# Performance work log

Hardware: AMD Instinct MI355X
Metric: run time of the kernel (lower is better)

## Reference

```python
import jax, jax.numpy as jnp
import numpy as np

B, C, H, W = 8, 256, 32, 32
N_HEADS, CH = 8, 32          # channel_head = channels // num_heads
HID = N_HEADS * CH           # hidden_channels


def setup_inputs() -> dict:
    key = jax.random.key(0)
    k1, k2, k3 = jax.random.split(key, 3)
    return {
        "x": jax.random.normal(k1, (B, C, H, W), dtype=jnp.float32),
        "w_qkv": jax.random.normal(k2, (3 * HID, C), dtype=jnp.float32) * 0.02,
        "b_qkv": jnp.zeros((3 * HID,), dtype=jnp.float32),
        "w_out": jax.random.normal(k3, (C, HID), dtype=jnp.float32) * 0.02,
        "b_out": jnp.zeros((C,), dtype=jnp.float32),
    }


def reference(x, w_qkv, b_qkv, w_out, b_out):
    b, c, h, w = x.shape
    s = h * w
    # qkv_conv: 1x1 conv + SiLU (norm='none' inside Conv2dBlock)
    qkv = jnp.einsum('bchw,oc->bohw', x, w_qkv) + b_qkv[None, :, None, None]
    qkv = jax.nn.silu(qkv)
    # rearrange 'b (n c) h w -> b n (3*ch) s' then chunk into q,k,v
    qkv = qkv.reshape(b, N_HEADS, 3 * CH, s)
    q, k, v = jnp.split(qkv, 3, axis=2)          # each [b, n, ch, s]
    # scores over flattened spatial positions, scaled by sqrt(channel_head)
    scores = jnp.einsum('bncs,bnct->bnst', q, k) / jnp.sqrt(jnp.float32(CH))
    attn = jax.nn.softmax(scores, axis=-1)        # softmax over key positions
    out = jnp.einsum('bnst,bnct->bncs', attn, v)  # [b, n, ch, s]
    out = out.reshape(b, N_HEADS * CH, h, w)      # 'b n c h w -> b (n c) h w'
    # out_conv: 1x1 conv, activation='none'
    out = jnp.einsum('bchw,oc->bohw', out, w_out) + b_out[None, :, None, None]
    # skip_connect=True, norm='none' => identity
    return out + x
```

## Files before the change

kernel.cpp:

```cpp
#include <hip/hip_runtime.h>
#include <math.h>

#define BB   8
#define NHD  8
#define SSZ  1024
#define CIN  256
#define HIDC 256

typedef __bf16 bf16_t;
typedef bf16_t bf16x8 __attribute__((ext_vector_type(8)));
typedef float  f32x4v __attribute__((ext_vector_type(4)));

typedef __attribute__((address_space(3))) unsigned short as3_u16;
typedef __attribute__((address_space(1))) unsigned short as1_u16;

__device__ inline unsigned cvt_pk_bf16(float lo, float hi) {
    unsigned r;
    asm("v_cvt_pk_bf16_f32 %0, %1, %2" : "=v"(r) : "v"(lo), "v"(hi));
    return r;
}
__device__ inline unsigned short f2bf(float f) {
    unsigned u = __builtin_bit_cast(unsigned, f);
    u = (u + 0x7fffu + ((u >> 16) & 1u)) >> 16;
    return (unsigned short)u;
}
__device__ inline float exp2_fast(float x) {
    float r;
    asm("v_exp_f32 %0, %1" : "=v"(r) : "v"(x));
    return r;
}
__device__ inline int kmap5(int i) {
    return ((i >> 2) & 3) * 8 + ((i >> 4) & 1) * 4 + (i & 3);
}

#define QKV_LDS_LOAD(WF, XF, KB)                                                    \
    {                                                                               \
        _Pragma("unroll") for (int df = 0; df < 3; ++df) {                          \
            const int orow = (w >> 1) * 48 + df * 16 + ln;                          \
            WF[df] = *(const bf16x8*)(Ws + orow * 128 + ((((KB) + g) ^ (orow & 15)) << 3)); \
        }                                                                           \
        _Pragma("unroll") for (int sf = 0; sf < 4; ++sf) {                          \
            const int srow = sbl + sf * 16 + ln;                                    \
            XF[sf] = *(const bf16x8*)(Xs + srow * 128 + ((((KB) + g) ^ (srow & 15)) << 3)); \
        }                                                                           \
    }
#define QKV_MMA(WF, XF)                                                             \
    {                                                                               \
        _Pragma("unroll") for (int df = 0; df < 3; ++df)                            \
            _Pragma("unroll") for (int sf = 0; sf < 4; ++sf)                        \
                acc[df][sf] = __builtin_amdgcn_mfma_f32_16x16x32_bf16(WF[df], XF[sf], acc[df][sf], 0, 0, 0); \
    }

__global__ __launch_bounds__(256) void qkv_fused(
    const float* __restrict__ W, const float* __restrict__ x,
    const float* __restrict__ w_out, const float* __restrict__ bias,
    unsigned short* __restrict__ qkT, unsigned short* __restrict__ v_buf,
    unsigned short* __restrict__ Wo)
{
    __shared__ unsigned short Ws[96 * 128];
    __shared__ unsigned short Xs[128 * 128];

    const int tid = threadIdx.x;

    if (blockIdx.y == 8) {
        const int chunk = blockIdx.z * 8 + blockIdx.x;
        const size_t idx = (size_t)chunk * 1024 + (size_t)tid * 4;
        float4 v = *(const float4*)(w_out + idx);
        ushort4 pk;
        pk.x = f2bf(v.x); pk.y = f2bf(v.y); pk.z = f2bf(v.z); pk.w = f2bf(v.w);
        *(ushort4*)(Wo + idx) = pk;
        return;
    }

    const int l = tid & 63, w = tid >> 6;
    const int g = l >> 4, ln = l & 15;
    const int b  = blockIdx.z;
    const int head = blockIdx.y;
    const int o0 = head * 96;
    const int ob = o0 + (w >> 1) * 48;
    const int s0 = blockIdx.x * 128;
    const int sbl = (w & 1) * 64;
    const int bh  = b * NHD + head;

    f32x4v acc[3][4];
    const f32x4v zero4 = {0.f, 0.f, 0.f, 0.f};
    #pragma unroll
    for (int df = 0; df < 3; ++df)
        #pragma unroll
        for (int sf = 0; sf < 4; ++sf) acc[df][sf] = zero4;

    bf16x8 wA[3], xA[4], wB[3], xB[4];

    #pragma unroll
    for (int h = 0; h < 2; ++h) {
        if (h) __syncthreads();
        #pragma unroll
        for (int it = 0; it < 12; ++it) {
            const int u   = it * 256 + tid;
            const int row = u >> 5;
            const int cq  = u & 31;
            const float4 v = *(const float4*)(W + (size_t)(o0 + row) * 256 + h * 128 + cq * 4);
            const int c_loc = cq * 4;
            const int cbp   = ((c_loc >> 3) ^ (row & 15)) << 3;
            unsigned two[2] = { cvt_pk_bf16(v.x, v.y), cvt_pk_bf16(v.z, v.w) };
            *(uint2*)(Ws + row * 128 + cbp + (c_loc & 7)) = *(uint2*)two;
        }
        #pragma unroll
        for (int it = 0; it < 8; ++it) {
            const int u  = it * 256 + tid;
            const int cp = u >> 5;
            const int sq = u & 31;
            const float* r0 = x + ((size_t)b * CIN + h * 128 + 2 * cp) * SSZ + s0 + sq * 4;
            const f32x4v a = *(const f32x4v*)r0;
            const f32x4v d = *(const f32x4v*)(r0 + SSZ);
            const int c_loc = 2 * cp;
            const int cb    = c_loc >> 3;
            #pragma unroll
            for (int j = 0; j < 4; ++j) {
                const int s_loc = sq * 4 + j;
                const int elem  = s_loc * 128 + ((cb ^ (s_loc & 15)) << 3) + (c_loc & 7);
                *(unsigned*)(Xs + elem) = cvt_pk_bf16(a[j], d[j]);
            }
        }
        __syncthreads();

        QKV_LDS_LOAD(wA, xA, 0);
        QKV_LDS_LOAD(wB, xB, 4);
        QKV_MMA(wA, xA);
        QKV_LDS_LOAD(wA, xA, 8);
        QKV_MMA(wB, xB);
        QKV_LDS_LOAD(wB, xB, 12);
        QKV_MMA(wA, xA);
        QKV_MMA(wB, xB);
    }

    #pragma unroll
    for (int df = 0; df < 3; ++df) {
        const int o16  = ob + df * 16;
        const int part = (o16 >> 5) % 3;
        const float4 b4 = *(const float4*)(bias + o16 + g * 4);
        const float bias_r[4] = {b4.x, b4.y, b4.z, b4.w};
        const int chb = (o16 & 31) + g * 4;

        float vals[4][4];
        #pragma unroll
        for (int sf = 0; sf < 4; ++sf)
            #pragma unroll
            for (int r = 0; r < 4; ++r) {
                float z = acc[df][sf][r] + bias_r[r];
                z = z / (1.f + __expf(-z));
                if (part == 0) z *= 0.25503482107810536f;
                vals[sf][r] = z;
            }

        if (part < 2) {
            const int slotb = ((chb >> 2) & 3) * 8 + ((chb >> 4) & 1) * 4;
            #pragma unroll
            for (int sf = 0; sf < 4; ++sf) {
                const int key = s0 + sbl + sf * 16 + ln;
                ushort4 pk;
                pk.x = f2bf(vals[sf][0]); pk.y = f2bf(vals[sf][1]);
                pk.z = f2bf(vals[sf][2]); pk.w = f2bf(vals[sf][3]);
                *(ushort4*)(qkT + ((size_t)bh << 16) + (size_t)key * 64 + part * 32 + slotb) = pk;
            }
        } else {
            #pragma unroll
            for (int sf = 0; sf < 4; ++sf) {
                const int key  = s0 + sbl + sf * 16 + ln;
                const int koff = (key & ~31) + kmap5(key & 31);
                #pragma unroll
                for (int r = 0; r < 4; ++r)
                    v_buf[((size_t)bh << 15) + ((size_t)(chb + r) << 10) + koff] = f2bf(vals[sf][r]);
            }
        }
    }
}

__global__ __launch_bounds__(256) void attn_mfma(
    const unsigned short* __restrict__ qkT,
    const unsigned short* __restrict__ v_buf,
    unsigned short* __restrict__ At)
{
    __shared__ unsigned short Ksh[4][2048];
    __shared__ unsigned short Vsh[4][2048];

    const int tid = threadIdx.x;
    const int l   = tid & 63;
    const int w   = tid >> 6;
    const int g   = l >> 4;
    const int ln  = l & 15;
    const int bh  = blockIdx.x;
    const int qt  = blockIdx.y;

    const unsigned short* qkrow = qkT   + ((size_t)bh << 16);
    const unsigned short* vb    = v_buf + ((size_t)bh << 15);

    const int q0 = qt * 64 + w * 16;

    const bf16x8 qf_ = *(const bf16x8*)(qkrow + (size_t)(q0 + ln) * 64 + g * 8);

    const bf16x8 ones = __builtin_bit_cast(bf16x8,
        make_uint4(0x3F803F80u, 0x3F803F80u, 0x3F803F80u, 0x3F803F80u));

    f32x4v O_[2], lacc;
    const f32x4v zero4 = {0.f, 0.f, 0.f, 0.f};
    O_[0] = zero4; O_[1] = zero4; lacc = zero4;

    const int krow = tid >> 2, ksl = tid & 3;
    const int vrow = tid >> 3, vsl = tid & 7;
    const unsigned short* gk_base = qkrow + (size_t)krow * 64 + 32 + ((ksl ^ ((krow >> 1) & 3)) << 3);
    const unsigned short* gv_base = vb + ((size_t)vrow << 10) + ((vsl ^ (vrow & 7)) << 3);
    const int wbase = w << 9;

#define STAGE_KV(BUF, T0)                                                          \
    {                                                                              \
        __builtin_amdgcn_global_load_lds((const as1_u16*)(gk_base + (size_t)(T0) * 64), \
                                         (as3_u16*)&Ksh[BUF][wbase], 16, 0, 0);    \
        __builtin_amdgcn_global_load_lds((const as1_u16*)(gv_base + (T0)),         \
                                         (as3_u16*)&Vsh[BUF][wbase], 16, 0, 0);    \
    }

    auto compute = [&](int cur) {
        const unsigned short* Kb = &Ksh[cur][0];
        const unsigned short* Vb = &Vsh[cur][0];
        bf16x8 kf_[4], vf_[2][2];
        #pragma unroll
        for (int kf = 0; kf < 4; ++kf)
            kf_[kf] = *(const bf16x8*)(Kb + ((kf * 16 + ln) << 5) + ((g ^ ((ln >> 1) & 3)) << 3));
        #pragma unroll
        for (int df = 0; df < 2; ++df)
            #pragma unroll
            for (int kb = 0; kb < 2; ++kb)
                vf_[df][kb] = *(const bf16x8*)(Vb + ((df * 16 + ln) << 6) + ((((kb << 2) + g) ^ (ln & 7)) << 3));

        f32x4v s_[4];
        __builtin_amdgcn_s_setprio(1);
        #pragma unroll
        for (int kf = 0; kf < 4; ++kf)
            s_[kf] = __builtin_amdgcn_mfma_f32_16x16x32_bf16(kf_[kf], qf_, zero4, 0, 0, 0);
        __builtin_amdgcn_s_setprio(0);

        #pragma unroll
        for (int kf = 0; kf < 4; ++kf)
            #pragma unroll
            for (int r = 0; r < 4; ++r)
                s_[kf][r] = exp2_fast(s_[kf][r]);

        __builtin_amdgcn_s_setprio(1);
        #pragma unroll
        for (int kb = 0; kb < 2; ++kb) {
            unsigned w0 = cvt_pk_bf16(s_[2 * kb][0],     s_[2 * kb][1]);
            unsigned w1 = cvt_pk_bf16(s_[2 * kb][2],     s_[2 * kb][3]);
            unsigned w2 = cvt_pk_bf16(s_[2 * kb + 1][0], s_[2 * kb + 1][1]);
            unsigned w3 = cvt_pk_bf16(s_[2 * kb + 1][2], s_[2 * kb + 1][3]);
            bf16x8 pf = __builtin_bit_cast(bf16x8, make_uint4(w0, w1, w2, w3));
            lacc = __builtin_amdgcn_mfma_f32_16x16x32_bf16(ones, pf, lacc, 0, 0, 0);
            #pragma unroll
            for (int df = 0; df < 2; ++df)
                O_[df] = __builtin_amdgcn_mfma_f32_16x16x32_bf16(vf_[df][kb], pf, O_[df], 0, 0, 0);
        }
        __builtin_amdgcn_s_setprio(0);
    };

    STAGE_KV(0, 0);
    STAGE_KV(1, 64);
    #pragma unroll
    for (int t = 0; t < 14; ++t) {
        STAGE_KV((t + 2) & 3, (t + 2) * 64);
        asm volatile("s_waitcnt vmcnt(4)" ::: "memory");
        __builtin_amdgcn_s_barrier();
        asm volatile("" ::: "memory");
        compute(t & 3);
        asm volatile("" ::: "memory");
    }
    asm volatile("s_waitcnt vmcnt(2)" ::: "memory");
    __builtin_amdgcn_s_barrier();
    asm volatile("" ::: "memory");
    compute(2);
    asm volatile("" ::: "memory");
    asm volatile("s_waitcnt vmcnt(0)" ::: "memory");
    __builtin_amdgcn_s_barrier();
    asm volatile("" ::: "memory");
    compute(3);

    const int b = bh >> 3, n = bh & 7;
    unsigned short* Ab = At + ((size_t)b << 18);
    const float inv = 1.f / lacc[0];
    const int qpos = q0 + ln;
    #pragma unroll
    for (int df = 0; df < 2; ++df) {
        ushort4 pk;
        pk.x = f2bf(O_[df][0] * inv);
        pk.y = f2bf(O_[df][1] * inv);
        pk.z = f2bf(O_[df][2] * inv);
        pk.w = f2bf(O_[df][3] * inv);
        *(ushort4*)(Ab + (size_t)qpos * 256 + n * 32 + df * 16 + g * 4) = pk;
    }
}

#define OUT_LOAD(WF, AF, KK)                                                        \
    {                                                                               \
        _Pragma("unroll") for (int df = 0; df < 2; ++df)                            \
            WF[df] = *(const bf16x8*)(Wo + (size_t)(ob + df * 16 + ln) * 256 + (KK) + g * 8); \
        _Pragma("unroll") for (int sf = 0; sf < 2; ++sf)                            \
            AF[sf] = *(const bf16x8*)(Ab + (size_t)(sb + sf * 16 + ln) * 256 + (KK) + g * 8); \
    }
#define OUT_MMA(WF, AF)                                                             \
    {                                                                               \
        _Pragma("unroll") for (int df = 0; df < 2; ++df)                            \
            _Pragma("unroll") for (int sf = 0; sf < 2; ++sf)                        \
                acc[df][sf] = __builtin_amdgcn_mfma_f32_16x16x32_bf16(WF[df], AF[sf], acc[df][sf], 0, 0, 0); \
    }

__global__ __launch_bounds__(256) void out_mfma(
    const unsigned short* __restrict__ Wo, const unsigned short* __restrict__ At,
    const float* __restrict__ bias, const float* __restrict__ x,
    float* __restrict__ out)
{
    const int tid = threadIdx.x;
    const int l = tid & 63, w = tid >> 6;
    const int g = l >> 4, ln = l & 15;
    const int b  = blockIdx.z;
    const int ob = blockIdx.y * 32;
    const int sb = blockIdx.x * 128 + w * 32;

    const unsigned short* Ab = At + ((size_t)b << 18);

    f32x4v acc[2][2];
    const f32x4v zero4 = {0.f, 0.f, 0.f, 0.f};
    #pragma unroll
    for (int df = 0; df < 2; ++df)
        #pragma unroll
        for (int sf = 0; sf < 2; ++sf) acc[df][sf] = zero4;

    bf16x8 wA[2], aA[2], wB[2], aB[2];
    OUT_LOAD(wA, aA, 0);
    #pragma unroll
    for (int k0 = 0; k0 < 256; k0 += 64) {
        if (k0 + 32 < 256) OUT_LOAD(wB, aB, k0 + 32);
        OUT_MMA(wA, aA);
        if (k0 + 64 < 256) OUT_LOAD(wA, aA, k0 + 64);
        OUT_MMA(wB, aB);
    }

    #pragma unroll
    for (int df = 0; df < 2; ++df) {
        const float4 b4 = *(const float4*)(bias + ob + df * 16 + g * 4);
        const float bias_r[4] = {b4.x, b4.y, b4.z, b4.w};
        #pragma unroll
        for (int sf = 0; sf < 2; ++sf) {
            const int s = sb + sf * 16 + ln;
            #pragma unroll
            for (int r = 0; r < 4; ++r) {
                const int o = ob + df * 16 + g * 4 + r;
                const size_t idx = ((size_t)b * CIN + o) * SSZ + s;
                out[idx] = acc[df][sf][r] + bias_r[r] + x[idx];
            }
        }
    }
}

extern "C" void kernel_launch(void* const* d_in, const int* in_sizes, int n_in,
                              void* d_out, int out_size, void* d_ws, size_t ws_size,
                              hipStream_t stream)
{
    const float* x     = (const float*)d_in[0];
    const float* w_qkv = (const float*)d_in[1];
    const float* b_qkv = (const float*)d_in[2];
    const float* w_out = (const float*)d_in[3];
    const float* b_out = (const float*)d_in[4];
    float* out = (float*)d_out;

    unsigned short* qkT   = (unsigned short*)d_ws;
    unsigned short* v_buf = qkT   + ((size_t)64 << 16);
    unsigned short* At    = v_buf + ((size_t)64 << 15);
    unsigned short* Wo    = At    + ((size_t)8 << 18);

    qkv_fused<<<dim3(8, 9, 8), 256, 0, stream>>>(w_qkv, x, w_out, b_qkv, qkT, v_buf, Wo);
    attn_mfma<<<dim3(64, 16),  256, 0, stream>>>(qkT, v_buf, At);
    out_mfma <<<dim3(8, 8, 8), 256, 0, stream>>>(Wo, At, b_out, x, out);
}
```

Baseline: 49.27 us.

## Split keys across wave pairs with 32-query tiles and LDS reduction in attention

Each wave now handles 32 queries (two 16-row fragments) and half of the key range, so each K/V fragment loaded from LDS feeds twice as many MFMAs. The block stages two key halves per step with double buffering, using 8 iterations instead of 16. A final LDS reduction combines the partial numerators and denominators across the two key halves. This adds extra barriers, per-lane register pressure and a reduction epilogue in exchange for less LDS fragment traffic per MFMA.

```diff
diff --git a/kernel.cpp b/kernel.cpp
--- a/kernel.cpp
+++ b/kernel.cpp
@@ -181,8 +181,8 @@
     const unsigned short* __restrict__ v_buf,
     unsigned short* __restrict__ At)
 {
-    __shared__ unsigned short Ksh[4][2048];
-    __shared__ unsigned short Vsh[4][2048];
+    __shared__ unsigned short Ksh[2][2][2048];
+    __shared__ unsigned short Vsh[2][2][2048];
 
     const int tid = threadIdx.x;
     const int l   = tid & 63;
@@ -191,20 +191,29 @@
     const int ln  = l & 15;
     const int bh  = blockIdx.x;
     const int qt  = blockIdx.y;
+    const int qgrp  = w >> 1;
+    const int khalf = w & 1;
 
     const unsigned short* qkrow = qkT   + ((size_t)bh << 16);
     const unsigned short* vb    = v_buf + ((size_t)bh << 15);
 
-    const int q0 = qt * 64 + w * 16;
-
-    const bf16x8 qf_ = *(const bf16x8*)(qkrow + (size_t)(q0 + ln) * 64 + g * 8);
+    const int q0 = qt * 64 + qgrp * 32;
+
+    bf16x8 qf_[2];
+    #pragma unroll
+    for (int qf = 0; qf < 2; ++qf)
+        qf_[qf] = *(const bf16x8*)(qkrow + (size_t)(q0 + qf * 16 + ln) * 64 + g * 8);
 
     const bf16x8 ones = __builtin_bit_cast(bf16x8,
         make_uint4(0x3F803F80u, 0x3F803F80u, 0x3F803F80u, 0x3F803F80u));
 
-    f32x4v O_[2], lacc;
+    f32x4v O_[2][2], lacc[2];
     const f32x4v zero4 = {0.f, 0.f, 0.f, 0.f};
-    O_[0] = zero4; O_[1] = zero4; lacc = zero4;
+    #pragma unroll
+    for (int df = 0; df < 2; ++df)
+        #pragma unroll
+        for (int qf = 0; qf < 2; ++qf) O_[df][qf] = zero4;
+    lacc[0] = zero4; lacc[1] = zero4;
 
     const int krow = tid >> 2, ksl = tid & 3;
     const int vrow = tid >> 3, vsl = tid & 7;
@@ -212,17 +221,20 @@
     const unsigned short* gv_base = vb + ((size_t)vrow << 10) + ((vsl ^ (vrow & 7)) << 3);
     const int wbase = w << 9;
 
-#define STAGE_KV(BUF, T0)                                                          \
+#define STAGE_PAIR(BUF, T)                                                         \
     {                                                                              \
-        __builtin_amdgcn_global_load_lds((const as1_u16*)(gk_base + (size_t)(T0) * 64), \
-                                         (as3_u16*)&Ksh[BUF][wbase], 16, 0, 0);    \
-        __builtin_amdgcn_global_load_lds((const as1_u16*)(gv_base + (T0)),         \
-                                         (as3_u16*)&Vsh[BUF][wbase], 16, 0, 0);    \
+        _Pragma("unroll") for (int hh = 0; hh < 2; ++hh) {                         \
+            const int koff = hh * 512 + (T) * 64;                                  \
+            __builtin_amdgcn_global_load_lds((const as1_u16*)(gk_base + (size_t)koff * 64), \
+                                             (as3_u16*)&Ksh[BUF][hh][wbase], 16, 0, 0); \
+            __builtin_amdgcn_global_load_lds((const as1_u16*)(gv_base + koff),    \
+                                             (as3_u16*)&Vsh[BUF][hh][wbase], 16, 0, 0); \
+        }                                                                          \
     }
 
     auto compute = [&](int cur) {
-        const unsigned short* Kb = &Ksh[cur][0];
-        const unsigned short* Vb = &Vsh[cur][0];
+        const unsigned short* Kb = &Ksh[cur][khalf][0];
+        const unsigned short* Vb = &Vsh[cur][khalf][0];
         bf16x8 kf_[4], vf_[2][2];
         #pragma unroll
         for (int kf = 0; kf < 4; ++kf)
@@ -233,68 +245,87 @@
             for (int kb = 0; kb < 2; ++kb)
                 vf_[df][kb] = *(const bf16x8*)(Vb + ((df * 16 + ln) << 6) + ((((kb << 2) + g) ^ (ln & 7)) << 3));
 
-        f32x4v s_[4];
-        __builtin_amdgcn_s_setprio(1);
-        #pragma unroll
-        for (int kf = 0; kf < 4; ++kf)
-            s_[kf] = __builtin_amdgcn_mfma_f32_16x16x32_bf16(kf_[kf], qf_, zero4, 0, 0, 0);
-        __builtin_amdgcn_s_setprio(0);
-
-        #pragma unroll
-        for (int kf = 0; kf < 4; ++kf)
-            #pragma unroll
-            for (int r = 0; r < 4; ++r)
-                s_[kf][r] = exp2_fast(s_[kf][r]);
-
-        __builtin_amdgcn_s_setprio(1);
-        #pragma unroll
-        for (int kb = 0; kb < 2; ++kb) {
-            unsigned w0 = cvt_pk_bf16(s_[2 * kb][0],     s_[2 * kb][1]);
-            unsigned w1 = cvt_pk_bf16(s_[2 * kb][2],     s_[2 * kb][3]);
-            unsigned w2 = cvt_pk_bf16(s_[2 * kb + 1][0], s_[2 * kb + 1][1]);
-            unsigned w3 = cvt_pk_bf16(s_[2 * kb + 1][2], s_[2 * kb + 1][3]);
-            bf16x8 pf = __builtin_bit_cast(bf16x8, make_uint4(w0, w1, w2, w3));
-            lacc = __builtin_amdgcn_mfma_f32_16x16x32_bf16(ones, pf, lacc, 0, 0, 0);
-            #pragma unroll
-            for (int df = 0; df < 2; ++df)
-                O_[df] = __builtin_amdgcn_mfma_f32_16x16x32_bf16(vf_[df][kb], pf, O_[df], 0, 0, 0);
-        }
-        __builtin_amdgcn_s_setprio(0);
+        #pragma unroll
+        for (int qf = 0; qf < 2; ++qf) {
+            f32x4v s_[4];
+            __builtin_amdgcn_s_setprio(1);
+            #pragma unroll
+            for (int kf = 0; kf < 4; ++kf)
+                s_[kf] = __builtin_amdgcn_mfma_f32_16x16x32_bf16(kf_[kf], qf_[qf], zero4, 0, 0, 0);
+            __builtin_amdgcn_s_setprio(0);
+
+            #pragma unroll
+            for (int kf = 0; kf < 4; ++kf)
+                #pragma unroll
+                for (int r = 0; r < 4; ++r)
+                    s_[kf][r] = exp2_fast(s_[kf][r]);
+
+            __builtin_amdgcn_s_setprio(1);
+            #pragma unroll
+            for (int kb = 0; kb < 2; ++kb) {
+                unsigned w0 = cvt_pk_bf16(s_[2 * kb][0],     s_[2 * kb][1]);
+                unsigned w1 = cvt_pk_bf16(s_[2 * kb][2],     s_[2 * kb][3]);
+                unsigned w2 = cvt_pk_bf16(s_[2 * kb + 1][0], s_[2 * kb + 1][1]);
+                unsigned w3 = cvt_pk_bf16(s_[2 * kb + 1][2], s_[2 * kb + 1][3]);
+                bf16x8 pf = __builtin_bit_cast(bf16x8, make_uint4(w0, w1, w2, w3));
+                lacc[qf] = __builtin_amdgcn_mfma_f32_16x16x32_bf16(ones, pf, lacc[qf], 0, 0, 0);
+                #pragma unroll
+                for (int df = 0; df < 2; ++df)
+                    O_[df][qf] = __builtin_amdgcn_mfma_f32_16x16x32_bf16(vf_[df][kb], pf, O_[df][qf], 0, 0, 0);
+            }
+            __builtin_amdgcn_s_setprio(0);
+        }
     };
 
-    STAGE_KV(0, 0);
-    STAGE_KV(1, 64);
-    #pragma unroll
-    for (int t = 0; t < 14; ++t) {
-        STAGE_KV((t + 2) & 3, (t + 2) * 64);
-        asm volatile("s_waitcnt vmcnt(4)" ::: "memory");
+    STAGE_PAIR(0, 0);
+    #pragma unroll
+    for (int t = 0; t < 8; ++t) {
+        if (t < 7) {
+            STAGE_PAIR((t + 1) & 1, t + 1);
+            asm volatile("s_waitcnt vmcnt(4)" ::: "memory");
+        } else {
+            asm volatile("s_waitcnt vmcnt(0)" ::: "memory");
+        }
         __builtin_amdgcn_s_barrier();
         asm volatile("" ::: "memory");
-        compute(t & 3);
+        compute(t & 1);
         asm volatile("" ::: "memory");
-    }
-    asm volatile("s_waitcnt vmcnt(2)" ::: "memory");
-    __builtin_amdgcn_s_barrier();
-    asm volatile("" ::: "memory");
-    compute(2);
-    asm volatile("" ::: "memory");
-    asm volatile("s_waitcnt vmcnt(0)" ::: "memory");
-    __builtin_amdgcn_s_barrier();
-    asm volatile("" ::: "memory");
-    compute(3);
-
-    const int b = bh >> 3, n = bh & 7;
-    unsigned short* Ab = At + ((size_t)b << 18);
-    const float inv = 1.f / lacc[0];
-    const int qpos = q0 + ln;
-    #pragma unroll
-    for (int df = 0; df < 2; ++df) {
-        ushort4 pk;
-        pk.x = f2bf(O_[df][0] * inv);
-        pk.y = f2bf(O_[df][1] * inv);
-        pk.z = f2bf(O_[df][2] * inv);
-        pk.w = f2bf(O_[df][3] * inv);
-        *(ushort4*)(Ab + (size_t)qpos * 256 + n * 32 + df * 16 + g * 4) = pk;
+        __builtin_amdgcn_s_barrier();
+    }
+
+    float* red = (float*)&Ksh[0][0][0];
+    float* myO = red + qgrp * 1152;
+    float* myl = myO + 1024;
+    if (khalf == 1) {
+        #pragma unroll
+        for (int df = 0; df < 2; ++df)
+            #pragma unroll
+            for (int qf = 0; qf < 2; ++qf)
+                #pragma unroll
+                for (int r = 0; r < 4; ++r)
+                    myO[((df * 2 + qf) * 4 + r) * 64 + l] = O_[df][qf][r];
+        #pragma unroll
+        for (int qf = 0; qf < 2; ++qf)
+            myl[qf * 64 + l] = lacc[qf][0];
+    }
+    __syncthreads();
+    if (khalf == 0) {
+        const int b = bh >> 3, n = bh & 7;
+        unsigned short* Ab = At + ((size_t)b << 18);
+        #pragma unroll
+        for (int qf = 0; qf < 2; ++qf) {
+            const float inv = 1.f / (lacc[qf][0] + myl[qf * 64 + l]);
+            const int qpos = q0 + qf * 16 + ln;
+            #pragma unroll
+            for (int df = 0; df < 2; ++df) {
+                ushort4 pk;
+                pk.x = f2bf((O_[df][qf][0] + myO[((df * 2 + qf) * 4 + 0) * 64 + l]) * inv);
+                pk.y = f2bf((O_[df][qf][1] + myO[((df * 2 + qf) * 4 + 1) * 64 + l]) * inv);
+                pk.z = f2bf((O_[df][qf][2] + myO[((df * 2 + qf) * 4 + 2) * 64 + l]) * inv);
+                pk.w = f2bf((O_[df][qf][3] + myO[((df * 2 + qf) * 4 + 3) * 64 + l]) * inv);
+                *(ushort4*)(Ab + (size_t)qpos * 256 + n * 32 + df * 16 + g * 4) = pk;
+            }
+        }
     }
 }
 
```

Measured after the change: 49.43 us. Within noise of the previous version (+0.3%).

## Prefetch second K-half of QKV operands into registers during first-half MFMA

Applied to the files above, without the earlier changes.

Splits the global-load-and-convert staging into separate register loads and LDS writes. The second half's W and x tiles are loaded into registers before the first half's MFMA loop, so global memory latency overlaps with compute. It also sets a minimum of two blocks per CU in launch bounds. The extra register buffers raise VGPR pressure and could cause spills or lower occupancy.

```diff
diff --git a/kernel.cpp b/kernel.cpp
--- a/kernel.cpp
+++ b/kernel.cpp
@@ -51,7 +51,7 @@
                 acc[df][sf] = __builtin_amdgcn_mfma_f32_16x16x32_bf16(WF[df], XF[sf], acc[df][sf], 0, 0, 0); \
     }
 
-__global__ __launch_bounds__(256) void qkv_fused(
+__global__ __launch_bounds__(256, 2) void qkv_fused(
     const float* __restrict__ W, const float* __restrict__ x,
     const float* __restrict__ w_out, const float* __restrict__ bias,
     unsigned short* __restrict__ qkT, unsigned short* __restrict__ v_buf,
@@ -82,6 +82,54 @@
     const int sbl = (w & 1) * 64;
     const int bh  = b * NHD + head;
 
+    f32x4v wbuf[12];
+    f32x4v xbuf[8][2];
+
+    auto load_w = [&](int h) {
+        #pragma unroll
+        for (int it = 0; it < 12; ++it) {
+            const int u = it * 256 + tid;
+            const int row = u >> 5, cq = u & 31;
+            wbuf[it] = *(const f32x4v*)(W + (size_t)(o0 + row) * 256 + h * 128 + cq * 4);
+        }
+    };
+    auto write_w = [&]() {
+        #pragma unroll
+        for (int it = 0; it < 12; ++it) {
+            const int u = it * 256 + tid;
+            const int row = u >> 5, cq = u & 31;
+            const int c_loc = cq * 4;
+            const int cbp = ((c_loc >> 3) ^ (row & 15)) << 3;
+            unsigned two[2] = { cvt_pk_bf16(wbuf[it][0], wbuf[it][1]),
+                                cvt_pk_bf16(wbuf[it][2], wbuf[it][3]) };
+            *(uint2*)(Ws + row * 128 + cbp + (c_loc & 7)) = *(uint2*)two;
+        }
+    };
+    auto load_x = [&](int h) {
+        #pragma unroll
+        for (int it = 0; it < 8; ++it) {
+            const int u = it * 256 + tid;
+            const int cp = u >> 5, sq = u & 31;
+            const float* r0 = x + ((size_t)b * CIN + h * 128 + 2 * cp) * SSZ + s0 + sq * 4;
+            xbuf[it][0] = *(const f32x4v*)r0;
+            xbuf[it][1] = *(const f32x4v*)(r0 + SSZ);
+        }
+    };
+    auto write_x = [&]() {
+        #pragma unroll
+        for (int it = 0; it < 8; ++it) {
+            const int u = it * 256 + tid;
+            const int cp = u >> 5, sq = u & 31;
+            const int c_loc = 2 * cp, cb = c_loc >> 3;
+            #pragma unroll
+            for (int j = 0; j < 4; ++j) {
+                const int s_loc = sq * 4 + j;
+                const int elem = s_loc * 128 + ((cb ^ (s_loc & 15)) << 3) + (c_loc & 7);
+                *(unsigned*)(Xs + elem) = cvt_pk_bf16(xbuf[it][0][j], xbuf[it][1][j]);
+            }
+        }
+    };
+
     f32x4v acc[3][4];
     const f32x4v zero4 = {0.f, 0.f, 0.f, 0.f};
     #pragma unroll
@@ -91,48 +139,33 @@
 
     bf16x8 wA[3], xA[4], wB[3], xB[4];
 
-    #pragma unroll
-    for (int h = 0; h < 2; ++h) {
-        if (h) __syncthreads();
-        #pragma unroll
-        for (int it = 0; it < 12; ++it) {
-            const int u   = it * 256 + tid;
-            const int row = u >> 5;
-            const int cq  = u & 31;
-            const float4 v = *(const float4*)(W + (size_t)(o0 + row) * 256 + h * 128 + cq * 4);
-            const int c_loc = cq * 4;
-            const int cbp   = ((c_loc >> 3) ^ (row & 15)) << 3;
-            unsigned two[2] = { cvt_pk_bf16(v.x, v.y), cvt_pk_bf16(v.z, v.w) };
-            *(uint2*)(Ws + row * 128 + cbp + (c_loc & 7)) = *(uint2*)two;
-        }
-        #pragma unroll
-        for (int it = 0; it < 8; ++it) {
-            const int u  = it * 256 + tid;
-            const int cp = u >> 5;
-            const int sq = u & 31;
-            const float* r0 = x + ((size_t)b * CIN + h * 128 + 2 * cp) * SSZ + s0 + sq * 4;
-            const f32x4v a = *(const f32x4v*)r0;
-            const f32x4v d = *(const f32x4v*)(r0 + SSZ);
-            const int c_loc = 2 * cp;
-            const int cb    = c_loc >> 3;
-            #pragma unroll
-            for (int j = 0; j < 4; ++j) {
-                const int s_loc = sq * 4 + j;
-                const int elem  = s_loc * 128 + ((cb ^ (s_loc & 15)) << 3) + (c_loc & 7);
-                *(unsigned*)(Xs + elem) = cvt_pk_bf16(a[j], d[j]);
-            }
-        }
-        __syncthreads();
-
-        QKV_LDS_LOAD(wA, xA, 0);
-        QKV_LDS_LOAD(wB, xB, 4);
-        QKV_MMA(wA, xA);
-        QKV_LDS_LOAD(wA, xA, 8);
-        QKV_MMA(wB, xB);
-        QKV_LDS_LOAD(wB, xB, 12);
-        QKV_MMA(wA, xA);
-        QKV_MMA(wB, xB);
-    }
+    load_w(0); load_x(0);
+    write_w(); write_x();
+    __syncthreads();
+
+    load_w(1); load_x(1);
+
+    QKV_LDS_LOAD(wA, xA, 0);
+    QKV_LDS_LOAD(wB, xB, 4);
+    QKV_MMA(wA, xA);
+    QKV_LDS_LOAD(wA, xA, 8);
+    QKV_MMA(wB, xB);
+    QKV_LDS_LOAD(wB, xB, 12);
+    QKV_MMA(wA, xA);
+    QKV_MMA(wB, xB);
+
+    __syncthreads();
+    write_w(); write_x();
+    __syncthreads();
+
+    QKV_LDS_LOAD(wA, xA, 0);
+    QKV_LDS_LOAD(wB, xB, 4);
+    QKV_MMA(wA, xA);
+    QKV_LDS_LOAD(wA, xA, 8);
+    QKV_MMA(wB, xB);
+    QKV_LDS_LOAD(wB, xB, 12);
+    QKV_MMA(wA, xA);
+    QKV_MMA(wB, xB);
 
     #pragma unroll
     for (int df = 0; df < 3; ++df) {
```

Result: slower. 50.38 us (+2.2%).
